# Kernel optimization log

Measured on AMD Instinct MI355X. Metric: run time of the kernel, lower is better.

Reference implementation:

```python
import jax, jax.numpy as jnp
import numpy as np

L, H, D = 4, 8, 256  # layers, heads, feature dim (Z has d+1 = 257 channels)
B, N1 = 8, 2048      # batch, N+1 tokens (N = 2047 context + 1 query)
STD = 0.02


def setup_inputs() -> dict:
    key = jax.random.key(0)
    k1, k2 = jax.random.split(key)
    Z = jax.random.normal(k1, (B, N1, D + 1), dtype=jnp.float32)
    allparam = STD * jax.random.normal(k2, (L, H, 2, D, D), dtype=jnp.float32)
    return {"Z": Z, "allparam": allparam}


def _attention(P, Q, Z):
    # P, Q: (d, d); Z: (B, N+1, d+1). act is None -> purely bilinear.
    Bn, N1_, d1 = Z.shape
    N, d = N1_ - 1, d1 - 1
    # Zero-padded (d+1, d+1) versions: P_full has a 1 in the label corner.
    P_full = jnp.zeros((d + 1, d + 1), Z.dtype).at[:d, :d].set(P).at[d, d].set(1.0)
    Q_full = jnp.zeros((d + 1, d + 1), Z.dtype).at[:d, :d].set(Q)
    sim = jnp.einsum('BNi,ij,BMj->BNM', Z, Q_full, Z)   # (B, N+1, N+1)
    val = jnp.einsum('ij,BNj->BNi', P_full, Z)            # (B, N+1, d+1)
    # A = eye(N+1) with A[N, N] = 0  ->  sim @ A @ val == sim @ (val with last token zeroed)
    val = val.at[:, N, :].set(0.0)
    return jnp.einsum('BNM,BMi->BNi', sim, val) / N


def reference(Z, allparam):
    for i in range(L):
        res = 0.0
        for j in range(H):  # small fixed head loop, matches torch structure
            P = allparam[i, j, 0]
            Q = allparam[i, j, 1]
            res = res + _attention(P, Q, Z)
        Z = Z + res
    return Z
```

## Files before the change

kernel.cpp:

```cpp
#include <hip/hip_runtime.h>


#define NL   4
#define NH   8
#define DD   256
#define NCH  257
#define NTOK 2048
#define NVAL 2047
#define NB   8

typedef short  short8v __attribute__((ext_vector_type(8)));
typedef short  short4v __attribute__((ext_vector_type(4)));
typedef float  f32x4   __attribute__((ext_vector_type(4)));

__device__ __forceinline__ unsigned short f2b(float x) {
  union { float f; unsigned u; } v; v.f = x;
  unsigned u = v.u + 0x7fffu + ((v.u >> 16) & 1u);
  return (unsigned short)(u >> 16);
}
__device__ __forceinline__ float b2f(short s) {
  union { unsigned u; float f; } v; v.u = ((unsigned)(unsigned short)s) << 16;
  return v.f;
}

__device__ __forceinline__ void mm64(const short* A, const short* B, int lda, int ldb,
                                     int ar, int bc, int k0, int k1, int lane,
                                     f32x4 (&acc)[4][4]) {
  #pragma unroll 2
  for (int kk = k0; kk < k1; kk += 32) {
    const int kc = kk + ((lane >> 4) << 3);
    short8v av[4], bv[4];
    #pragma unroll
    for (int f = 0; f < 4; ++f)
      av[f] = *(const short8v*)(A + (size_t)(ar + f * 16 + (lane & 15)) * lda + kc);
    #pragma unroll
    for (int g = 0; g < 4; ++g)
      bv[g] = *(const short8v*)(B + (size_t)(bc + g * 16 + (lane & 15)) * ldb + kc);
    #pragma unroll
    for (int f = 0; f < 4; ++f)
      #pragma unroll
      for (int g = 0; g < 4; ++g)
        acc[f][g] = __builtin_amdgcn_mfma_f32_16x16x32_bf16(av[f], bv[g], acc[f][g], 0, 0, 0);
  }
}

__global__ __launch_bounds__(256) void k_init(const float* __restrict__ Zin,
                                              const float* __restrict__ ap,
                                              short* __restrict__ Pbf, short* __restrict__ Qcat2,
                                              float* __restrict__ QsumT,
                                              short* __restrict__ Zxbf, short* __restrict__ Zxt,
                                              float* __restrict__ zlab) {
  __shared__ float lds[64][65];
  const int bx = blockIdx.x, tid = threadIdx.x;
  if (bx < 1024) {
    const f32x4* src = (const f32x4*)ap;
    int q0 = (bx * 256 + tid) * 2;
    #pragma unroll
    for (int u = 0; u < 2; ++u) {
      int q = q0 + u, lj = q >> 14, rc4 = q & 16383;
      f32x4 v = src[(size_t)(lj * 2) * 16384 + rc4];
      short4v o;
      #pragma unroll
      for (int i = 0; i < 4; ++i) o[i] = (short)f2b(v[i]);
      ((short4v*)Pbf)[(size_t)lj * 16384 + rc4] = o;
    }
    return;
  }
  if (bx < 2048) {
    int idx = bx - 1024;
    int l = idx >> 8, k = idx & 255;
    int j = tid >> 5, t0 = (tid & 31) * 8;
    const float* s = ap + (size_t)((l * 8 + j) * 2 + 1) * 65536 + (size_t)k * 256 + t0;
    f32x4 a = *(const f32x4*)s, bq = *(const f32x4*)(s + 4);
    short8v o;
    #pragma unroll
    for (int i = 0; i < 4; ++i) { o[i] = (short)f2b(a[i]); o[4 + i] = (short)f2b(bq[i]); }
    *(short8v*)(Qcat2 + (size_t)(l * 256 + k) * 2048 + j * 256 + t0) = o;
    return;
  }
  if (bx < 2112) {
    int qb = bx - 2048;
    int l = qb >> 4, xx = qb & 15;
    int k0 = (xx >> 2) * 64, t0 = (xx & 3) * 64;
    int c = tid & 63, r = tid >> 6;
    #pragma unroll
    for (int i = 0; i < 16; ++i) {
      int k = r + i * 4;
      float s = 0.f;
      #pragma unroll
      for (int j = 0; j < 8; ++j)
        s += ap[(size_t)((l * 8 + j) * 2 + 1) * 65536 + (size_t)(k0 + k) * 256 + (t0 + c)];
      lds[k][c] = s;
    }
    __syncthreads();
    #pragma unroll
    for (int i = 0; i < 16; ++i) {
      int tl = r + i * 4;
      QsumT[(size_t)l * 65536 + (size_t)(t0 + tl) * 256 + (k0 + c)] = lds[c][tl];
    }
    return;
  }
  int tb = bx - 2112;
  int x = tb & 3, y = (tb >> 2) & 31, b = tb >> 7;
  int k0 = x * 64, m0 = y * 64;
  int c = tid & 63, r = tid >> 6;
  #pragma unroll
  for (int i = 0; i < 16; ++i) {
    int mrow = r + i * 4, m = m0 + mrow;
    float v = Zin[((size_t)b * NTOK + m) * NCH + k0 + c];
    lds[mrow][c] = v;
    Zxbf[((size_t)b * NTOK + m) * DD + k0 + c] = (short)f2b(v);
  }
  if (x == 0 && tid < 64) {
    int m = m0 + tid;
    zlab[b * NTOK + m] = (m == NVAL) ? 0.f : Zin[((size_t)b * NTOK + m) * NCH + DD];
  }
  __syncthreads();
  #pragma unroll
  for (int i = 0; i < 16; ++i) {
    int krow = r + i * 4;
    float v = lds[c][krow];
    if (m0 + c == NVAL) v = 0.f;
    Zxt[((size_t)b * DD + k0 + krow) * NTOK + m0 + c] = (short)f2b(v);
  }
}

__global__ __launch_bounds__(256) void k_gram(const short* __restrict__ Zxt,
                                              const short* __restrict__ Zxbf,
                                              const float* __restrict__ zlab,
                                              float* __restrict__ Gacc,
                                              float* __restrict__ gcolacc) {
  __shared__ float zl[256];
  const int x = blockIdx.x, tid = threadIdx.x;
  if (x >= 512) {
    const int idx = x - 512, b = idx & 7, seg = idx >> 3;
    zl[tid] = zlab[b * NTOK + seg * 256 + tid];
    __syncthreads();
    const short* base = Zxbf + ((size_t)b * NTOK + seg * 256) * DD + tid;
    float s = 0.f;
    #pragma unroll 8
    for (int m = 0; m < 256; ++m) s += b2f(base[(size_t)m * DD]) * zl[m];
    gcolacc[(seg * 8 + b) * 256 + tid] = s;
    return;
  }
  const int lane = tid & 63, wid = tid >> 6;
  const int b = x & 7, t = (x >> 3) & 3, seg = x >> 5;
  const int r0 = (t >> 1) * 128, c0 = (t & 1) * 128;
  const int ar = r0 + (wid >> 1) * 64, bc = c0 + (wid & 1) * 64;
  const short* A = Zxt + (size_t)b * DD * NTOK;
  f32x4 acc[4][4];
  #pragma unroll
  for (int f = 0; f < 4; ++f) for (int g = 0; g < 4; ++g) for (int i = 0; i < 4; ++i) acc[f][g][i] = 0.f;
  mm64(A, A, NTOK, NTOK, ar, bc, seg * 128, seg * 128 + 128, lane, acc);
  float* out = Gacc + (size_t)(seg * 8 + b) * 65536;
  #pragma unroll
  for (int f = 0; f < 4; ++f)
    #pragma unroll
    for (int g = 0; g < 4; ++g)
      #pragma unroll
      for (int i = 0; i < 4; ++i)
        out[(size_t)(ar + f * 16 + ((lane >> 4) << 2) + i) * 256 + bc + g * 16 + (lane & 15)] = acc[f][g][i];
}

__global__ __launch_bounds__(256) void k_gred(const float* __restrict__ Gacc,
                                              const float* __restrict__ gcolacc,
                                              short* __restrict__ Gbf, float* __restrict__ gcol) {
  const int x = blockIdx.x, tid = threadIdx.x;
  if (x >= 512) {
    const int b = x - 512;
    float s = 0.f;
    #pragma unroll
    for (int seg = 0; seg < 8; ++seg) s += gcolacc[(seg * 8 + b) * 256 + tid];
    gcol[b * 256 + tid] = s;
    return;
  }
  const int i0 = (x * 256 + tid) * 4;
  const int b = i0 >> 16, el = i0 & 65535;
  f32x4 s = {0.f, 0.f, 0.f, 0.f};
  #pragma unroll
  for (int seg = 0; seg < 16; ++seg) {
    f32x4 v = *(const f32x4*)(Gacc + (size_t)(seg * 8 + b) * 65536 + el);
    #pragma unroll
    for (int i = 0; i < 4; ++i) s[i] += v[i];
  }
  short4v o;
  #pragma unroll
  for (int i = 0; i < 4; ++i) o[i] = (short)f2b(s[i]);
  *(short4v*)(Gbf + (size_t)b * 65536 + el) = o;
}

__global__ __launch_bounds__(256) void k_pv(const short* __restrict__ Gbf, const short* __restrict__ Pbf,
                                            const float* __restrict__ QsumT, const float* __restrict__ gcol,
                                            short* __restrict__ Vt3, float* __restrict__ mcol, int layer) {
  __shared__ float gs[256];
  const int x = blockIdx.x, tid = threadIdx.x;
  if (x >= 256) {
    const int b = x - 256;
    gs[tid] = gcol[b * 256 + tid];
    __syncthreads();
    float s = 0.f;
    for (int t = 0; t < 256; ++t) s += QsumT[(size_t)layer * 65536 + (size_t)t * 256 + tid] * gs[t];
    mcol[b * 256 + tid] = s * (1.0f / (float)NVAL);
    return;
  }
  const int lane = tid & 63, wid = tid >> 6;
  const int b = x & 7, t = x >> 3;
  const int r0 = (t & 1) * 128, c0 = (t >> 1) * 128;
  const int ar = r0 + (wid >> 1) * 64, bc = c0 + (wid & 1) * 64;
  const short* A = Gbf + (size_t)b * 65536;
  const short* B = Pbf + (size_t)layer * 8 * 65536;
  f32x4 acc[4][4];
  #pragma unroll
  for (int f = 0; f < 4; ++f) for (int g = 0; g < 4; ++g) for (int i = 0; i < 4; ++i) acc[f][g][i] = 0.f;
  mm64(A, B, 256, 256, ar, bc, 0, 256, lane, acc);
  short* out = Vt3 + (size_t)b * 524288;
  #pragma unroll
  for (int f = 0; f < 4; ++f) {
    const int tt0 = ar + f * 16 + ((lane >> 4) << 2);
    #pragma unroll
    for (int g = 0; g < 4; ++g) {
      const int jc = bc + g * 16 + (lane & 15);
      const int j = jc >> 8, c = jc & 255;
      short4v p;
      #pragma unroll
      for (int i = 0; i < 4; ++i) p[i] = (short)f2b(acc[f][g][i]);
      *(short4v*)(out + (size_t)c * 2048 + j * 256 + tt0) = p;
    }
  }
}

__global__ __launch_bounds__(256) void k_qm(const short* __restrict__ Vt3, const short* __restrict__ Qcat2,
                                            float* __restrict__ Macc, int layer) {
  const int x = blockIdx.x, tid = threadIdx.x;
  const int lane = tid & 63, wid = tid >> 6;
  const int b = x & 7, t = (x >> 3) & 3, seg = x >> 5;
  const int r0 = (t >> 1) * 128, c0 = (t & 1) * 128;
  const int ar = r0 + (wid >> 1) * 64, bc = c0 + (wid & 1) * 64;
  const short* A = Vt3 + (size_t)b * 524288;
  const short* B = Qcat2 + (size_t)layer * 524288;
  f32x4 acc[4][4];
  #pragma unroll
  for (int f = 0; f < 4; ++f) for (int g = 0; g < 4; ++g) for (int i = 0; i < 4; ++i) acc[f][g][i] = 0.f;
  mm64(A, B, 2048, 2048, ar, bc, seg * 128, seg * 128 + 128, lane, acc);
  float* out = Macc + (size_t)(seg * 8 + b) * 65536;
  #pragma unroll
  for (int f = 0; f < 4; ++f)
    #pragma unroll
    for (int g = 0; g < 4; ++g)
      #pragma unroll
      for (int i = 0; i < 4; ++i)
        out[(size_t)(ar + f * 16 + ((lane >> 4) << 2) + i) * 256 + bc + g * 16 + (lane & 15)] = acc[f][g][i];
}

__global__ __launch_bounds__(256) void k_mred(const float* __restrict__ Macc, short* __restrict__ Mt) {
  const int x = blockIdx.x, tid = threadIdx.x;
  const int i0 = (x * 256 + tid) * 4;
  const int b = i0 >> 16, el = i0 & 65535;
  f32x4 s = {0.f, 0.f, 0.f, 0.f};
  #pragma unroll
  for (int seg = 0; seg < 16; ++seg) {
    f32x4 v = *(const f32x4*)(Macc + (size_t)(seg * 8 + b) * 65536 + el);
    #pragma unroll
    for (int i = 0; i < 4; ++i) s[i] += v[i];
  }
  const float invN = 1.0f / (float)NVAL;
  short4v o;
  #pragma unroll
  for (int i = 0; i < 4; ++i) o[i] = (short)f2b(s[i] * invN);
  *(short4v*)(Mt + (size_t)b * 65536 + el) = o;
}

__global__ __launch_bounds__(256) void k_apply(const float* __restrict__ Zsrc, float* __restrict__ Z,
                                               const short* __restrict__ Zxin, const short* __restrict__ Mt,
                                               const float* __restrict__ mcol,
                                               short* __restrict__ Zxout, short* __restrict__ Zxt_out,
                                               float* __restrict__ zlab_out, int wnext) {
  __shared__ short ldsT[128][136];
  const int tid = threadIdx.x, lane = tid & 63, wid = tid >> 6;
  const int wr = wid >> 1, wc = wid & 1;
  const int x = blockIdx.x;
  const int b = x & 7, t = x >> 3;
  const int ar_wg = (t >> 1) * 128, bc_wg = (t & 1) * 128;
  const int ar = ar_wg + wr * 64, bc = bc_wg + wc * 64;
  const short* A = Zxin + (size_t)b * NTOK * DD;
  const short* B = Mt + (size_t)b * 65536;
  const bool gemv = ((t & 1) == 0 && wc == 0);
  f32x4 acc[4][4];
  #pragma unroll
  for (int f = 0; f < 4; ++f) for (int g = 0; g < 4; ++g) for (int i = 0; i < 4; ++i) acc[f][g][i] = 0.f;
  float s[4] = {0.f, 0.f, 0.f, 0.f};
  #pragma unroll 2
  for (int kk = 0; kk < 256; kk += 32) {
    const int kc = kk + ((lane >> 4) << 3);
    short8v av[4], bv[4];
    #pragma unroll
    for (int f = 0; f < 4; ++f)
      av[f] = *(const short8v*)(A + (size_t)(ar + f * 16 + (lane & 15)) * DD + kc);
    #pragma unroll
    for (int g = 0; g < 4; ++g)
      bv[g] = *(const short8v*)(B + (size_t)(bc + g * 16 + (lane & 15)) * 256 + kc);
    if (gemv) {
      const float* mp = mcol + b * 256 + kc;
      f32x4 m0 = *(const f32x4*)mp, m1 = *(const f32x4*)(mp + 4);
      #pragma unroll
      for (int f = 0; f < 4; ++f) {
        #pragma unroll
        for (int q = 0; q < 4; ++q) {
          s[f] += b2f(av[f][q]) * m0[q];
          s[f] += b2f(av[f][4 + q]) * m1[q];
        }
      }
    }
    #pragma unroll
    for (int f = 0; f < 4; ++f)
      #pragma unroll
      for (int g = 0; g < 4; ++g)
        acc[f][g] = __builtin_amdgcn_mfma_f32_16x16x32_bf16(av[f], bv[g], acc[f][g], 0, 0, 0);
  }
  #pragma unroll
  for (int f = 0; f < 4; ++f) {
    const int nb = ar + f * 16 + ((lane >> 4) << 2);
    #pragma unroll
    for (int g = 0; g < 4; ++g) {
      const int c = bc + g * 16 + (lane & 15);
      #pragma unroll
      for (int i = 0; i < 4; ++i) {
        size_t idx = ((size_t)b * NTOK + nb + i) * NCH + c;
        float nv = Zsrc[idx] + acc[f][g][i];
        Z[idx] = nv;
        unsigned short bvv = f2b(nv);
        if (wnext) {
          Zxout[((size_t)b * NTOK + nb + i) * DD + c] = (short)bvv;
          ldsT[c - bc_wg][nb - ar_wg + i] = (nb + i == NVAL) ? (short)0 : (short)bvv;
        }
      }
    }
  }
  if (gemv) {
    #pragma unroll
    for (int f = 0; f < 4; ++f) {
      float tt = s[f];
      tt += __shfl_xor(tt, 16);
      tt += __shfl_xor(tt, 32);
      if ((lane >> 4) == 0) {
        int n = ar + f * 16 + (lane & 15);
        size_t idx = ((size_t)b * NTOK + n) * NCH + DD;
        float nv = Zsrc[idx] + tt;
        Z[idx] = nv;
        if (wnext) zlab_out[b * NTOK + n] = (n == NVAL) ? 0.f : nv;
      }
    }
  }
  if (wnext) {
    __syncthreads();
    const int n0 = (tid & 15) * 8, cr0 = (tid >> 4) * 8;
    #pragma unroll
    for (int r = 0; r < 8; ++r) {
      short8v v = *(const short8v*)&ldsT[cr0 + r][n0];
      *(short8v*)(Zxt_out + ((size_t)b * DD + bc_wg + cr0 + r) * NTOK + ar_wg + n0) = v;
    }
  }
}

extern "C" void kernel_launch(void* const* d_in, const int* in_sizes, int n_in,
                              void* d_out, int out_size, void* d_ws, size_t ws_size,
                              hipStream_t stream) {
  const float* Zin      = (const float*)d_in[0];
  const float* allparam = (const float*)d_in[1];
  float* Z = (float*)d_out;

  const size_t o_zx0  = 0;
  const size_t o_zx1  = o_zx0  + 8388608;
  const size_t o_zxt  = o_zx1  + 8388608;
  const size_t o_acc  = o_zxt  + 8388608;
  const size_t o_gbf  = o_acc  + 33554432;
  const size_t o_vt   = o_gbf  + 1048576;
  const size_t o_mt   = o_vt   + 8388608;
  const size_t o_pbf  = o_mt   + 1048576;
  const size_t o_qc2  = o_pbf  + 4194304;
  const size_t o_qsum = o_qc2  + 4194304;
  const size_t o_gca  = o_qsum + 1048576;
  const size_t o_gcol = o_gca  + 65536;
  const size_t o_mcol = o_gcol + 8192;
  const size_t o_zlab = o_mcol + 8192;
  const size_t NEED   = o_zlab + 65536;
  if (ws_size < NEED) return;

  char* wsb = (char*)d_ws;
  short* Zx[2]   = { (short*)(wsb + o_zx0), (short*)(wsb + o_zx1) };
  short* Zxt     = (short*)(wsb + o_zxt);
  float* Acc     = (float*)(wsb + o_acc);
  short* Gbf     = (short*)(wsb + o_gbf);
  short* Vt3     = (short*)(wsb + o_vt);
  short* Mt      = (short*)(wsb + o_mt);
  short* Pbf     = (short*)(wsb + o_pbf);
  short* Qcat2   = (short*)(wsb + o_qc2);
  float* QsumT   = (float*)(wsb + o_qsum);
  float* gcolacc = (float*)(wsb + o_gca);
  float* gcol    = (float*)(wsb + o_gcol);
  float* mcol    = (float*)(wsb + o_mcol);
  float* zlab    = (float*)(wsb + o_zlab);

  k_init<<<dim3(3136), dim3(256), 0, stream>>>(Zin, allparam, Pbf, Qcat2, QsumT,
                                               Zx[0], Zxt, zlab);

  for (int layer = 0; layer < NL; ++layer) {
    const int cur = layer & 1;
    const int wnext = (layer < NL - 1) ? 1 : 0;
    const float* Zsrc = (layer == 0) ? Zin : Z;
    k_gram<<<dim3(576), dim3(256), 0, stream>>>(Zxt, Zx[cur], zlab, Acc, gcolacc);
    k_gred<<<dim3(520), dim3(256), 0, stream>>>(Acc, gcolacc, Gbf, gcol);
    k_pv<<<dim3(264), dim3(256), 0, stream>>>(Gbf, Pbf, QsumT, gcol, Vt3, mcol, layer);
    k_qm<<<dim3(512), dim3(256), 0, stream>>>(Vt3, Qcat2, Acc, layer);
    k_mred<<<dim3(512), dim3(256), 0, stream>>>(Acc, Mt);
    k_apply<<<dim3(256), dim3(256), 0, stream>>>(Zsrc, Z, Zx[cur], Mt, mcol,
                                                 Zx[cur ^ 1], Zxt, zlab, wnext);
  }
}
```

Before: 400.3 us.

## Store split-K partials in bf16 and drop precomputed QsumT

```diff
diff --git a/kernel.cpp b/kernel.cpp
--- a/kernel.cpp
+++ b/kernel.cpp
@@ -47,7 +47,6 @@
 __global__ __launch_bounds__(256) void k_init(const float* __restrict__ Zin,
                                               const float* __restrict__ ap,
                                               short* __restrict__ Pbf, short* __restrict__ Qcat2,
-                                              float* __restrict__ QsumT,
                                               short* __restrict__ Zxbf, short* __restrict__ Zxt,
                                               float* __restrict__ zlab) {
   __shared__ float lds[64][65];
@@ -78,29 +77,7 @@
     *(short8v*)(Qcat2 + (size_t)(l * 256 + k) * 2048 + j * 256 + t0) = o;
     return;
   }
-  if (bx < 2112) {
-    int qb = bx - 2048;
-    int l = qb >> 4, xx = qb & 15;
-    int k0 = (xx >> 2) * 64, t0 = (xx & 3) * 64;
-    int c = tid & 63, r = tid >> 6;
-    #pragma unroll
-    for (int i = 0; i < 16; ++i) {
-      int k = r + i * 4;
-      float s = 0.f;
-      #pragma unroll
-      for (int j = 0; j < 8; ++j)
-        s += ap[(size_t)((l * 8 + j) * 2 + 1) * 65536 + (size_t)(k0 + k) * 256 + (t0 + c)];
-      lds[k][c] = s;
-    }
-    __syncthreads();
-    #pragma unroll
-    for (int i = 0; i < 16; ++i) {
-      int tl = r + i * 4;
-      QsumT[(size_t)l * 65536 + (size_t)(t0 + tl) * 256 + (k0 + c)] = lds[c][tl];
-    }
-    return;
-  }
-  int tb = bx - 2112;
+  int tb = bx - 2048;
   int x = tb & 3, y = (tb >> 2) & 31, b = tb >> 7;
   int k0 = x * 64, m0 = y * 64;
   int c = tid & 63, r = tid >> 6;
@@ -128,7 +105,7 @@
 __global__ __launch_bounds__(256) void k_gram(const short* __restrict__ Zxt,
                                               const short* __restrict__ Zxbf,
                                               const float* __restrict__ zlab,
-                                              float* __restrict__ Gacc,
+                                              short* __restrict__ Gacc,
                                               float* __restrict__ gcolacc) {
   __shared__ float zl[256];
   const int x = blockIdx.x, tid = threadIdx.x;
@@ -152,45 +129,50 @@
   #pragma unroll
   for (int f = 0; f < 4; ++f) for (int g = 0; g < 4; ++g) for (int i = 0; i < 4; ++i) acc[f][g][i] = 0.f;
   mm64(A, A, NTOK, NTOK, ar, bc, seg * 128, seg * 128 + 128, lane, acc);
-  float* out = Gacc + (size_t)(seg * 8 + b) * 65536;
-  #pragma unroll
-  for (int f = 0; f < 4; ++f)
-    #pragma unroll
-    for (int g = 0; g < 4; ++g)
-      #pragma unroll
-      for (int i = 0; i < 4; ++i)
-        out[(size_t)(ar + f * 16 + ((lane >> 4) << 2) + i) * 256 + bc + g * 16 + (lane & 15)] = acc[f][g][i];
-}
-
-__global__ __launch_bounds__(256) void k_gred(const float* __restrict__ Gacc,
+  short* out = Gacc + (size_t)(seg * 8 + b) * 65536;
+  #pragma unroll
+  for (int f = 0; f < 4; ++f) {
+    const int rb = ar + f * 16 + ((lane >> 4) << 2);
+    #pragma unroll
+    for (int g = 0; g < 4; ++g) {
+      const int col = bc + g * 16 + (lane & 15);
+      short4v p;
+      #pragma unroll
+      for (int i = 0; i < 4; ++i) p[i] = (short)f2b(acc[f][g][i]);
+      *(short4v*)(out + (size_t)col * 256 + rb) = p;
+    }
+  }
+}
+
+__global__ __launch_bounds__(256) void k_gred(const short* __restrict__ Gacc,
                                               const float* __restrict__ gcolacc,
                                               short* __restrict__ Gbf, float* __restrict__ gcol) {
   const int x = blockIdx.x, tid = threadIdx.x;
-  if (x >= 512) {
-    const int b = x - 512;
+  if (x >= 256) {
+    const int b = x - 256;
     float s = 0.f;
     #pragma unroll
     for (int seg = 0; seg < 8; ++seg) s += gcolacc[(seg * 8 + b) * 256 + tid];
     gcol[b * 256 + tid] = s;
     return;
   }
-  const int i0 = (x * 256 + tid) * 4;
-  const int b = i0 >> 16, el = i0 & 65535;
-  f32x4 s = {0.f, 0.f, 0.f, 0.f};
+  const int b = x & 7, chunk = x >> 3;
+  const int i0 = chunk * 2048 + tid * 8;
+  float s[8] = {};
   #pragma unroll
   for (int seg = 0; seg < 16; ++seg) {
-    f32x4 v = *(const f32x4*)(Gacc + (size_t)(seg * 8 + b) * 65536 + el);
-    #pragma unroll
-    for (int i = 0; i < 4; ++i) s[i] += v[i];
-  }
-  short4v o;
-  #pragma unroll
-  for (int i = 0; i < 4; ++i) o[i] = (short)f2b(s[i]);
-  *(short4v*)(Gbf + (size_t)b * 65536 + el) = o;
+    short8v v = *(const short8v*)(Gacc + (size_t)(seg * 8 + b) * 65536 + i0);
+    #pragma unroll
+    for (int q = 0; q < 8; ++q) s[q] += b2f(v[q]);
+  }
+  short8v o;
+  #pragma unroll
+  for (int q = 0; q < 8; ++q) o[q] = (short)f2b(s[q]);
+  *(short8v*)(Gbf + (size_t)b * 65536 + i0) = o;
 }
 
 __global__ __launch_bounds__(256) void k_pv(const short* __restrict__ Gbf, const short* __restrict__ Pbf,
-                                            const float* __restrict__ QsumT, const float* __restrict__ gcol,
+                                            const short* __restrict__ Qcat2, const float* __restrict__ gcol,
                                             short* __restrict__ Vt3, float* __restrict__ mcol, int layer) {
   __shared__ float gs[256];
   const int x = blockIdx.x, tid = threadIdx.x;
@@ -198,8 +180,13 @@
     const int b = x - 256;
     gs[tid] = gcol[b * 256 + tid];
     __syncthreads();
+    const short* qrow = Qcat2 + (size_t)layer * 524288 + (size_t)tid * 2048;
     float s = 0.f;
-    for (int t = 0; t < 256; ++t) s += QsumT[(size_t)layer * 65536 + (size_t)t * 256 + tid] * gs[t];
+    for (int jt = 0; jt < 2048; jt += 8) {
+      short8v v = *(const short8v*)(qrow + jt);
+      #pragma unroll
+      for (int q = 0; q < 8; ++q) s += b2f(v[q]) * gs[(jt + q) & 255];
+    }
     mcol[b * 256 + tid] = s * (1.0f / (float)NVAL);
     return;
   }
@@ -230,44 +217,49 @@
 }
 
 __global__ __launch_bounds__(256) void k_qm(const short* __restrict__ Vt3, const short* __restrict__ Qcat2,
-                                            float* __restrict__ Macc, int layer) {
+                                            short* __restrict__ Macc, int layer) {
   const int x = blockIdx.x, tid = threadIdx.x;
   const int lane = tid & 63, wid = tid >> 6;
   const int b = x & 7, t = (x >> 3) & 3, seg = x >> 5;
   const int r0 = (t >> 1) * 128, c0 = (t & 1) * 128;
   const int ar = r0 + (wid >> 1) * 64, bc = c0 + (wid & 1) * 64;
-  const short* A = Vt3 + (size_t)b * 524288;
-  const short* B = Qcat2 + (size_t)layer * 524288;
+  const short* A = Qcat2 + (size_t)layer * 524288;
+  const short* B = Vt3 + (size_t)b * 524288;
   f32x4 acc[4][4];
   #pragma unroll
   for (int f = 0; f < 4; ++f) for (int g = 0; g < 4; ++g) for (int i = 0; i < 4; ++i) acc[f][g][i] = 0.f;
   mm64(A, B, 2048, 2048, ar, bc, seg * 128, seg * 128 + 128, lane, acc);
-  float* out = Macc + (size_t)(seg * 8 + b) * 65536;
-  #pragma unroll
-  for (int f = 0; f < 4; ++f)
-    #pragma unroll
-    for (int g = 0; g < 4; ++g)
-      #pragma unroll
-      for (int i = 0; i < 4; ++i)
-        out[(size_t)(ar + f * 16 + ((lane >> 4) << 2) + i) * 256 + bc + g * 16 + (lane & 15)] = acc[f][g][i];
-}
-
-__global__ __launch_bounds__(256) void k_mred(const float* __restrict__ Macc, short* __restrict__ Mt) {
+  short* out = Macc + (size_t)(seg * 8 + b) * 65536;
+  #pragma unroll
+  for (int f = 0; f < 4; ++f) {
+    const int kb = ar + f * 16 + ((lane >> 4) << 2);
+    #pragma unroll
+    for (int g = 0; g < 4; ++g) {
+      const int c = bc + g * 16 + (lane & 15);
+      short4v p;
+      #pragma unroll
+      for (int i = 0; i < 4; ++i) p[i] = (short)f2b(acc[f][g][i]);
+      *(short4v*)(out + (size_t)c * 256 + kb) = p;
+    }
+  }
+}
+
+__global__ __launch_bounds__(256) void k_mred(const short* __restrict__ Macc, short* __restrict__ Mt) {
   const int x = blockIdx.x, tid = threadIdx.x;
-  const int i0 = (x * 256 + tid) * 4;
-  const int b = i0 >> 16, el = i0 & 65535;
-  f32x4 s = {0.f, 0.f, 0.f, 0.f};
+  const int b = x & 7, chunk = x >> 3;
+  const int i0 = chunk * 2048 + tid * 8;
+  float s[8] = {};
   #pragma unroll
   for (int seg = 0; seg < 16; ++seg) {
-    f32x4 v = *(const f32x4*)(Macc + (size_t)(seg * 8 + b) * 65536 + el);
-    #pragma unroll
-    for (int i = 0; i < 4; ++i) s[i] += v[i];
+    short8v v = *(const short8v*)(Macc + (size_t)(seg * 8 + b) * 65536 + i0);
+    #pragma unroll
+    for (int q = 0; q < 8; ++q) s[q] += b2f(v[q]);
   }
   const float invN = 1.0f / (float)NVAL;
-  short4v o;
-  #pragma unroll
-  for (int i = 0; i < 4; ++i) o[i] = (short)f2b(s[i] * invN);
-  *(short4v*)(Mt + (size_t)b * 65536 + el) = o;
+  short8v o;
+  #pragma unroll
+  for (int q = 0; q < 8; ++q) o[q] = (short)f2b(s[q] * invN);
+  *(short8v*)(Mt + (size_t)b * 65536 + i0) = o;
 }
 
 __global__ __launch_bounds__(256) void k_apply(const float* __restrict__ Zsrc, float* __restrict__ Z,
@@ -373,13 +365,12 @@
   const size_t o_zx1  = o_zx0  + 8388608;
   const size_t o_zxt  = o_zx1  + 8388608;
   const size_t o_acc  = o_zxt  + 8388608;
-  const size_t o_gbf  = o_acc  + 33554432;
+  const size_t o_gbf  = o_acc  + 16777216;
   const size_t o_vt   = o_gbf  + 1048576;
   const size_t o_mt   = o_vt   + 8388608;
   const size_t o_pbf  = o_mt   + 1048576;
   const size_t o_qc2  = o_pbf  + 4194304;
-  const size_t o_qsum = o_qc2  + 4194304;
-  const size_t o_gca  = o_qsum + 1048576;
+  const size_t o_gca  = o_qc2  + 4194304;
   const size_t o_gcol = o_gca  + 65536;
   const size_t o_mcol = o_gcol + 8192;
   const size_t o_zlab = o_mcol + 8192;
@@ -389,30 +380,28 @@
   char* wsb = (char*)d_ws;
   short* Zx[2]   = { (short*)(wsb + o_zx0), (short*)(wsb + o_zx1) };
   short* Zxt     = (short*)(wsb + o_zxt);
-  float* Acc     = (float*)(wsb + o_acc);
+  short* Acc     = (short*)(wsb + o_acc);
   short* Gbf     = (short*)(wsb + o_gbf);
   short* Vt3     = (short*)(wsb + o_vt);
   short* Mt      = (short*)(wsb + o_mt);
   short* Pbf     = (short*)(wsb + o_pbf);
   short* Qcat2   = (short*)(wsb + o_qc2);
-  float* QsumT   = (float*)(wsb + o_qsum);
   float* gcolacc = (float*)(wsb + o_gca);
   float* gcol    = (float*)(wsb + o_gcol);
   float* mcol    = (float*)(wsb + o_mcol);
   float* zlab    = (float*)(wsb + o_zlab);
 
-  k_init<<<dim3(3136), dim3(256), 0, stream>>>(Zin, allparam, Pbf, Qcat2, QsumT,
-                                               Zx[0], Zxt, zlab);
+  k_init<<<dim3(3072), dim3(256), 0, stream>>>(Zin, allparam, Pbf, Qcat2, Zx[0], Zxt, zlab);
 
   for (int layer = 0; layer < NL; ++layer) {
     const int cur = layer & 1;
     const int wnext = (layer < NL - 1) ? 1 : 0;
     const float* Zsrc = (layer == 0) ? Zin : Z;
     k_gram<<<dim3(576), dim3(256), 0, stream>>>(Zxt, Zx[cur], zlab, Acc, gcolacc);
-    k_gred<<<dim3(520), dim3(256), 0, stream>>>(Acc, gcolacc, Gbf, gcol);
-    k_pv<<<dim3(264), dim3(256), 0, stream>>>(Gbf, Pbf, QsumT, gcol, Vt3, mcol, layer);
+    k_gred<<<dim3(264), dim3(256), 0, stream>>>(Acc, gcolacc, Gbf, gcol);
+    k_pv<<<dim3(264), dim3(256), 0, stream>>>(Gbf, Pbf, Qcat2, gcol, Vt3, mcol, layer);
     k_qm<<<dim3(512), dim3(256), 0, stream>>>(Vt3, Qcat2, Acc, layer);
-    k_mred<<<dim3(512), dim3(256), 0, stream>>>(Acc, Mt);
+    k_mred<<<dim3(256), dim3(256), 0, stream>>>(Acc, Mt);
     k_apply<<<dim3(256), dim3(256), 0, stream>>>(Zsrc, Z, Zx[cur], Mt, mcol,
                                                  Zx[cur ^ 1], Zxt, zlab, wnext);
   }
```

Measured after the change: 465.5 us. +16.3%, slower.
